# Kernel optimization log

Hardware: AMD Instinct MI355X
Metric: run time of the kernel (lower is better)

## Reference

```python
import jax, jax.numpy as jnp
import numpy as np
from jax import lax

B, Hs, Ws = 2, 256, 256
DIM = 256        # query channels (c)
DIM_BAK = 256    # key/value channels (c2)
HEADS = 8
WIN = 8
HEAD_DIM = DIM // HEADS
SCALE = HEAD_DIM ** -0.5


def window_partition(x, ws):
    # x: [B, H, W, C] -> [B*nH*nW, ws, ws, C]
    b, h, w, c = x.shape
    x = x.reshape(b, h // ws, ws, w // ws, ws, c)
    return x.transpose(0, 1, 3, 2, 4, 5).reshape(-1, ws, ws, c)


def window_reverse(windows, ws, h, w):
    # windows: [B*nH*nW, ws, ws, C] -> [B, H, W, C]
    b = windows.shape[0] // ((h // ws) * (w // ws))
    x = windows.reshape(b, h // ws, w // ws, ws, ws, -1)
    return x.transpose(0, 1, 3, 2, 4, 5).reshape(b, h, w, -1)


def setup_inputs() -> dict:
    key = jax.random.key(0)
    ks = jax.random.split(key, 9)
    s = 0.02
    return {
        "query_feature": jax.random.normal(ks[0], (B, DIM, Hs, Ws), jnp.float32),
        "key_value_feature": jax.random.normal(ks[1], (B, DIM_BAK, Hs, Ws), jnp.float32),
        # depthwise 3x3 conv on kv (groups=DIM_BAK, bias=False): OIHW with I=1
        "w_dw": jax.random.normal(ks[2], (DIM_BAK, 1, 3, 3), jnp.float32) * s,
        # to_q: Linear(dim -> dim), stored [in, out]
        "wq": jax.random.normal(ks[3], (DIM, DIM), jnp.float32) * s,
        "bq": jax.random.normal(ks[4], (DIM,), jnp.float32) * s,
        # to_kv: Linear(dim_bak -> 2*dim)
        "wkv": jax.random.normal(ks[5], (DIM_BAK, 2 * DIM), jnp.float32) * s,
        "bkv": jax.random.normal(ks[6], (2 * DIM,), jnp.float32) * s,
        # project_out: Linear(dim -> dim)
        "w_proj": jax.random.normal(ks[7], (DIM, DIM), jnp.float32) * s,
        "b_proj": jax.random.normal(ks[8], (DIM,), jnp.float32) * s,
    }


def reference(query_feature, key_value_feature, w_dw, wq, bq, wkv, bkv, w_proj, b_proj):
    b, c, h, w = query_feature.shape
    c2 = key_value_feature.shape[1]

    # depthwise 3x3 conv on key/value feature (padding=1, stride=1)
    kv = lax.conv_general_dilated(
        key_value_feature, w_dw,
        window_strides=(1, 1), padding="SAME",
        feature_group_count=c2,
        dimension_numbers=("NCHW", "OIHW", "NCHW"))

    # NCHW -> NHWC, partition into non-overlapping windows
    qw = window_partition(query_feature.transpose(0, 2, 3, 1), WIN)  # [B_, ws, ws, c]
    kvw = window_partition(kv.transpose(0, 2, 3, 1), WIN)            # [B_, ws, ws, c2]
    B_ = qw.shape[0]
    N = WIN * WIN
    qw = qw.reshape(B_, N, c)
    kvw = kvw.reshape(B_, N, c2)

    # projections -> multi-head [B_, heads, N, head_dim]
    q = (qw @ wq + bq).reshape(B_, N, HEADS, HEAD_DIM).transpose(0, 2, 1, 3) * SCALE
    kv_proj = (kvw @ wkv + bkv).reshape(B_, N, 2, HEADS, HEAD_DIM)
    k = kv_proj[:, :, 0].transpose(0, 2, 1, 3)
    v = kv_proj[:, :, 1].transpose(0, 2, 1, 3)

    # windowed cross-attention
    attn = jax.nn.softmax(jnp.einsum("bhnd,bhmd->bhnm", q, k), axis=-1)
    out = jnp.einsum("bhnm,bhmd->bhnd", attn, v)
    out = out.transpose(0, 2, 1, 3).reshape(B_, N, c)
    out = out @ w_proj + b_proj

    # reverse windows, back to NCHW
    out = window_reverse(out.reshape(B_, WIN, WIN, c), WIN, h, w)
    return out.transpose(0, 3, 1, 2)
```

## Files before the change

### kernel.cpp

```cpp
#include <hip/hip_runtime.h>
#include <hip/hip_bf16.h>
#include <cstdint>
#include <cstddef>

typedef __hip_bfloat16 bf16;
typedef short bf16x8 __attribute__((ext_vector_type(8)));
typedef float f32x4 __attribute__((ext_vector_type(4)));

#define MFMA(a, b, c) __builtin_amdgcn_mfma_f32_16x16x32_bf16((a), (b), (c), 0, 0, 0)

__global__ __launch_bounds__(256) void wtrans_k(const float* __restrict__ wq,
                                                const float* __restrict__ wkv,
                                                const float* __restrict__ wp,
                                                bf16* __restrict__ wqT,
                                                bf16* __restrict__ wkvT,
                                                bf16* __restrict__ wpT) {
  int idx = blockIdx.x * 256 + threadIdx.x;
  if (idx < 65536) {
    int n = idx >> 8, k = idx & 255;
    wqT[idx] = __float2bfloat16(wq[k * 256 + n]);
  } else if (idx < 196608) {
    int i = idx - 65536;
    int n = i >> 8, k = i & 255;
    wkvT[i] = __float2bfloat16(wkv[k * 512 + n]);
  } else {
    int i = idx - 196608;
    int n = i >> 8, k = i & 255;
    wpT[i] = __float2bfloat16(wp[k * 256 + n]);
  }
}

__global__ __launch_bounds__(256) void t_winq_k(const float* __restrict__ src,
                                                bf16* __restrict__ dst,
                                                int hw0, int swoff) {
  __shared__ bf16 T[64][66];
  int tile = blockIdx.x;
  int c0 = (tile & 3) << 6;
  int hwb = hw0 + ((tile >> 2) << 6);
  int tid = threadIdx.x;
  {
    int hwl = tid & 63, cb = tid >> 6;
    const float* s = src + (size_t)(c0 + cb) * 65536 + hwb + hwl;
#pragma unroll
    for (int i = 0; i < 16; ++i)
      T[cb + i * 4][hwl] = __float2bfloat16(s[(size_t)i * 4 * 65536]);
  }
  __syncthreads();
  {
    int cl = tid & 63, hb = tid >> 6;
#pragma unroll
    for (int j = 0; j < 16; ++j) {
      int hwl = hb + j * 4;
      int hw = hwb + hwl;
      int h = hw >> 8, w = hw & 255;
      int sw = swoff + ((h >> 3) << 5) + (w >> 3);
      int t = ((h & 7) << 3) + (w & 7);
      dst[((size_t)(sw * 64 + t) << 8) + c0 + cl] = T[cl][hwl];
    }
  }
}

__global__ __launch_bounds__(256) void t_nhwc_k(const float* __restrict__ src,
                                                bf16* __restrict__ dst) {
  __shared__ bf16 T[64][66];
  int tile = blockIdx.x;
  int c0 = (tile & 3) << 6;
  int hwoff = (tile >> 2) << 6;
  int tid = threadIdx.x;
  {
    int hwl = tid & 63, cb = tid >> 6;
    const float* s = src + (size_t)(c0 + cb) * 65536 + hwoff + hwl;
#pragma unroll
    for (int i = 0; i < 16; ++i)
      T[cb + i * 4][hwl] = __float2bfloat16(s[(size_t)i * 4 * 65536]);
  }
  __syncthreads();
  {
    int cl = tid & 63, hb = tid >> 6;
#pragma unroll
    for (int j = 0; j < 16; ++j) {
      int hwl = hb + j * 4;
      dst[((size_t)(hwoff + hwl) << 8) + c0 + cl] = T[cl][hwl];
    }
  }
}

__global__ __launch_bounds__(256) void convkv_k(const bf16* __restrict__ SK,
                                                const float* __restrict__ wdw,
                                                const bf16* __restrict__ wkvT,
                                                const float* __restrict__ bkv,
                                                bf16* __restrict__ k_s,
                                                bf16* __restrict__ vT_s,
                                                int wid_base, int cnt, int psw0,
                                                int nwtot) {
  __shared__ __align__(16) bf16 X[64 * 256];
  auto xp = [&](int row, int col) -> bf16* {
    int by = (row << 9) + (col << 1);
    by ^= (row & 7) << 4;
    return (bf16*)((char*)X + by);
  };
  int bid = blockIdx.x;
  int swc = (bid & 7) * (cnt >> 3) + (bid >> 3);
  int sw = psw0 + swc;
  int wid = wid_base + swc;
  int rem = wid & 1023, wh = rem >> 5, ww = rem & 31;
  int h0 = wh * 8, w0 = ww * 8;
  int tid = threadIdx.x;
  {
    int c = tid;
    float wr[9];
#pragma unroll
    for (int q = 0; q < 9; ++q) wr[q] = wdw[c * 9 + q];
    const bool wlo = (w0 > 0), whi = (w0 < 248);
    float rows[3][10];
    auto load_row = [&](int gh, float* r) {
      if (gh >= 0 && gh < 256) {
        const bf16* rp = SK + ((size_t)(gh * 256 + w0) << 8) + c;
        r[0] = wlo ? __bfloat162float(rp[-256]) : 0.f;
#pragma unroll
        for (int s = 1; s <= 8; ++s) r[s] = __bfloat162float(rp[(s - 1) * 256]);
        r[9] = whi ? __bfloat162float(rp[8 * 256]) : 0.f;
      } else {
#pragma unroll
        for (int e = 0; e < 10; ++e) r[e] = 0.f;
      }
    };
    load_row(h0 - 1, rows[0]);
    load_row(h0, rows[1]);
#pragma unroll
    for (int i = 0; i < 8; ++i) {
      load_row(h0 + i + 1, rows[(i + 2) % 3]);
#pragma unroll
      for (int j = 0; j < 8; ++j) {
        float acc = 0.f;
#pragma unroll
        for (int di = 0; di < 3; ++di) {
          const float* rp = rows[(i + di) % 3];
          acc = __builtin_fmaf(wr[di * 3 + 0], rp[j], acc);
          acc = __builtin_fmaf(wr[di * 3 + 1], rp[j + 1], acc);
          acc = __builtin_fmaf(wr[di * 3 + 2], rp[j + 2], acc);
        }
        *xp(i * 8 + j, c) = __float2bfloat16(acc);
      }
    }
  }
  __syncthreads();
  int wave = tid >> 6, lane = tid & 63, quad = lane >> 4, l16 = lane & 15;
  int n0 = wave * 64;
  f32x4 zero4 = {0.f, 0.f, 0.f, 0.f};
  f32x4 acc[4][4];
  for (int mt = 0; mt < 4; ++mt)
    for (int nt = 0; nt < 4; ++nt) acc[mt][nt] = zero4;
  for (int k0 = 0; k0 < 256; k0 += 32) {
    bf16x8 a[4], bb[4];
    for (int mt = 0; mt < 4; ++mt)
      a[mt] = *(const bf16x8*)xp(mt * 16 + l16, k0 + quad * 8);
    for (int nt = 0; nt < 4; ++nt)
      bb[nt] = *(const bf16x8*)&wkvT[(size_t)(n0 + nt * 16 + l16) * 256 + k0 + quad * 8];
    for (int mt = 0; mt < 4; ++mt)
      for (int nt = 0; nt < 4; ++nt) acc[mt][nt] = MFMA(a[mt], bb[nt], acc[mt][nt]);
  }
  for (int nt = 0; nt < 4; ++nt) {
    int n = n0 + nt * 16 + l16;
    float bias = bkv[n];
    for (int mt = 0; mt < 4; ++mt) {
      int mb = mt * 16 + quad * 4;
      for (int r = 0; r < 4; ++r)
        k_s[((size_t)(sw * 64 + mb + r) << 8) + n] =
            __float2bfloat16(acc[mt][nt][r] + bias);
    }
  }
  for (int mt = 0; mt < 4; ++mt)
    for (int nt = 0; nt < 4; ++nt) acc[mt][nt] = zero4;
  for (int k0 = 0; k0 < 256; k0 += 32) {
    bf16x8 a[4], bb[4];
    for (int mt = 0; mt < 4; ++mt)
      a[mt] = *(const bf16x8*)xp(mt * 16 + l16, k0 + quad * 8);
    for (int nt = 0; nt < 4; ++nt)
      bb[nt] = *(const bf16x8*)&wkvT[(size_t)(256 + n0 + nt * 16 + l16) * 256 + k0 + quad * 8];
    for (int mt = 0; mt < 4; ++mt)
      for (int nt = 0; nt < 4; ++nt) acc[mt][nt] = MFMA(bb[nt], a[mt], acc[mt][nt]);
  }
  for (int nt = 0; nt < 4; ++nt) {
    for (int r = 0; r < 4; ++r) {
      int vd = n0 + nt * 16 + quad * 4 + r;
      float bias = bkv[256 + vd];
      for (int mt = 0; mt < 4; ++mt)
        vT_s[((size_t)(sw * 256 + vd) << 6) + mt * 16 + l16] =
            __float2bfloat16(acc[mt][nt][r] + bias);
    }
  }
}

__global__ __launch_bounds__(256, 3) void fused_k(const bf16* __restrict__ qwM,
                                                  const bf16* __restrict__ wqT,
                                                  const float* __restrict__ bq,
                                                  const bf16* __restrict__ k_s,
                                                  const bf16* __restrict__ vT_s,
                                                  const bf16* __restrict__ wpT,
                                                  const float* __restrict__ bp,
                                                  float* __restrict__ out,
                                                  int wid_base, int nw) {
  __shared__ __align__(16) bf16 LA[4 * 64 * 64];
  __shared__ __align__(16) bf16 LB[4 * 64 * 32];
  int bid = blockIdx.x;
  int sw = (bid & 7) * (nw >> 3) + (bid >> 3);
  int wid = wid_base + sw;
  int b = wid >> 10, rem = wid & 1023, wh = rem >> 5, ww = rem & 31;
  int h0 = wh * 8, w0 = ww * 8;
  int tid = threadIdx.x, wave = tid >> 6, lane = tid & 63, quad = lane >> 4, l16 = lane & 15;
  char* Abase = (char*)LA + wave * 8192;
  char* Bbase = (char*)LB + wave * 4096;
  auto apR = [&](int w, int row, int col) -> bf16* {
    int by = (row << 7) + (col << 1);
    by ^= (row & 7) << 4;
    return (bf16*)((char*)LA + w * 8192 + by);
  };
  auto ap = [&](int row, int col) -> bf16* {
    int by = (row << 7) + (col << 1);
    by ^= (row & 7) << 4;
    return (bf16*)(Abase + by);
  };
  auto Bp = [&](int row, int col) -> bf16* {
    int by = (row << 6) + (col << 1);
    by ^= (row & 3) << 4;
    return (bf16*)(Bbase + by);
  };
  f32x4 zero4 = {0.f, 0.f, 0.f, 0.f};
  {
    const bf16* Aq = qwM + ((size_t)sw << 14);
    f32x4 acc[4][4];
    for (int mt = 0; mt < 4; ++mt)
      for (int nt = 0; nt < 4; ++nt) acc[mt][nt] = zero4;
    for (int k0 = 0; k0 < 256; k0 += 32) {
      bf16x8 a[4], bb[4];
      for (int mt = 0; mt < 4; ++mt)
        a[mt] = *(const bf16x8*)&Aq[(size_t)(mt * 16 + l16) * 256 + k0 + quad * 8];
      for (int nt = 0; nt < 4; ++nt) {
        int n = (wave + ((nt >> 1) << 2)) * 32 + (nt & 1) * 16 + l16;
        bb[nt] = *(const bf16x8*)&wqT[(size_t)n * 256 + k0 + quad * 8];
      }
      for (int mt = 0; mt < 4; ++mt)
        for (int nt = 0; nt < 4; ++nt) acc[mt][nt] = MFMA(a[mt], bb[nt], acc[mt][nt]);
    }
    const float scale = 0.1767766952966369f;
    for (int nt = 0; nt < 4; ++nt) {
      int n = (wave + ((nt >> 1) << 2)) * 32 + (nt & 1) * 16 + l16;
      float bias = bq[n];
      for (int mt = 0; mt < 4; ++mt) {
        int mb = mt * 16 + quad * 4;
        for (int r = 0; r < 4; ++r)
          *ap(mb + r, nt * 16 + l16) =
              __float2bfloat16((acc[mt][nt][r] + bias) * scale);
      }
    }
  }
  const bf16* kw = k_s + ((size_t)sw << 14);
  const bf16* vw = vT_s + ((size_t)sw << 14);
  for (int hi = 0; hi < 2; ++hi) {
    int co = (wave + hi * 4) * 32;
    int lc = hi * 32;
    f32x4 s[4][4];
    for (int mt = 0; mt < 4; ++mt)
      for (int nt = 0; nt < 4; ++nt) s[mt][nt] = zero4;
    {
      bf16x8 a[4], bb[4];
      for (int mt = 0; mt < 4; ++mt)
        a[mt] = *(const bf16x8*)ap(mt * 16 + l16, lc + quad * 8);
      for (int nt = 0; nt < 4; ++nt)
        bb[nt] = *(const bf16x8*)&kw[(size_t)(nt * 16 + l16) * 256 + co + quad * 8];
      for (int mt = 0; mt < 4; ++mt)
        for (int nt = 0; nt < 4; ++nt) s[mt][nt] = MFMA(a[mt], bb[nt], s[mt][nt]);
    }
    float rsum[4][4];
    for (int mt = 0; mt < 4; ++mt) {
      for (int r = 0; r < 4; ++r) {
        float m = s[mt][0][r];
        for (int nt = 1; nt < 4; ++nt) m = fmaxf(m, s[mt][nt][r]);
        m = fmaxf(m, __shfl_xor(m, 1, 64));
        m = fmaxf(m, __shfl_xor(m, 2, 64));
        m = fmaxf(m, __shfl_xor(m, 4, 64));
        m = fmaxf(m, __shfl_xor(m, 8, 64));
        float sum = 0.f;
        for (int nt = 0; nt < 4; ++nt) {
          float e = __expf(s[mt][nt][r] - m);
          s[mt][nt][r] = e;
          sum += e;
        }
        sum += __shfl_xor(sum, 1, 64);
        sum += __shfl_xor(sum, 2, 64);
        sum += __shfl_xor(sum, 4, 64);
        sum += __shfl_xor(sum, 8, 64);
        rsum[mt][r] = sum;
      }
    }
    f32x4 o[4][2];
    for (int mt = 0; mt < 4; ++mt)
      for (int nt = 0; nt < 2; ++nt) o[mt][nt] = zero4;
    for (int half = 0; half < 2; ++half) {
      for (int mt = 0; mt < 4; ++mt)
        for (int nt2 = 0; nt2 < 2; ++nt2)
          for (int r = 0; r < 4; ++r)
            *Bp(mt * 16 + quad * 4 + r, nt2 * 16 + l16) =
                __float2bfloat16(s[mt][half * 2 + nt2][r]);
      bf16x8 pa[4], vb[2];
      for (int mt = 0; mt < 4; ++mt)
        pa[mt] = *(const bf16x8*)Bp(mt * 16 + l16, quad * 8);
      for (int nt = 0; nt < 2; ++nt)
        vb[nt] = *(const bf16x8*)&vw[(size_t)(co + nt * 16 + l16) * 64 + half * 32 + quad * 8];
      for (int mt = 0; mt < 4; ++mt)
        for (int nt = 0; nt < 2; ++nt) o[mt][nt] = MFMA(pa[mt], vb[nt], o[mt][nt]);
    }
    for (int mt = 0; mt < 4; ++mt) {
      int mb = mt * 16 + quad * 4;
      for (int nt = 0; nt < 2; ++nt)
        for (int r = 0; r < 4; ++r)
          *ap(mb + r, lc + nt * 16 + l16) =
              __float2bfloat16(o[mt][nt][r] / rsum[mt][r]);
    }
  }
  __syncthreads();
  {
    int n0 = wave * 64;
    f32x4 acc[4][4];
    for (int mt = 0; mt < 4; ++mt)
      for (int nt = 0; nt < 4; ++nt) acc[mt][nt] = zero4;
    for (int k0 = 0; k0 < 256; k0 += 32) {
      int head = k0 >> 5;
      int rw = head & 3;
      int lc = (head >> 2) * 32;
      bf16x8 a[4], bb[4];
      for (int mt = 0; mt < 4; ++mt)
        a[mt] = *(const bf16x8*)apR(rw, mt * 16 + l16, lc + quad * 8);
      for (int nt = 0; nt < 4; ++nt)
        bb[nt] = *(const bf16x8*)&wpT[(size_t)(n0 + nt * 16 + l16) * 256 + k0 + quad * 8];
      for (int mt = 0; mt < 4; ++mt)
        for (int nt = 0; nt < 4; ++nt) acc[mt][nt] = MFMA(a[mt], bb[nt], acc[mt][nt]);
    }
    for (int nt = 0; nt < 4; ++nt) {
      int n = n0 + nt * 16 + l16;
      float bias = bp[n];
      float* chan = out + ((size_t)(b * 256 + n) << 16);
      for (int mt = 0; mt < 4; ++mt) {
        int row_i = mt * 2 + (quad >> 1);
        int j0 = (quad & 1) * 4;
        f32x4 v4;
        for (int r = 0; r < 4; ++r) v4[r] = acc[mt][nt][r] + bias;
        *(f32x4*)&chan[(size_t)(h0 + row_i) * 256 + w0 + j0] = v4;
      }
    }
  }
}

extern "C" void kernel_launch(void* const* d_in, const int* in_sizes, int n_in,
                              void* d_out, int out_size, void* d_ws, size_t ws_size,
                              hipStream_t stream) {
  const float* qf  = (const float*)d_in[0];
  const float* kvf = (const float*)d_in[1];
  const float* wdw = (const float*)d_in[2];
  const float* wq  = (const float*)d_in[3];
  const float* bq  = (const float*)d_in[4];
  const float* wkv = (const float*)d_in[5];
  const float* bkv = (const float*)d_in[6];
  const float* wp  = (const float*)d_in[7];
  const float* bp  = (const float*)d_in[8];
  float* out = (float*)d_out;

  bf16* wqT  = (bf16*)d_ws;
  bf16* wkvT = wqT + 65536;
  bf16* wpT  = wkvT + 131072;
  bf16* bufs = wpT + 65536;
  const size_t welems = 65536 + 131072 + 65536;
  const size_t skelems = (size_t)256 * 256 * 256;

  int passes = 1;
  while (passes < 32) {
    size_t nw_ = 2048 / passes;
    size_t elems = welems + skelems + 3 * nw_ * 16384;
    if (elems * 2 <= ws_size) break;
    passes <<= 1;
  }
  int nw = 2048 / passes;
  size_t sz = (size_t)nw * 16384;
  bf16* SK  = bufs;
  bf16* qwM = SK + skelems;
  bf16* KS  = qwM + sz;
  bf16* VT  = KS + sz;

  wtrans_k<<<1024, 256, 0, stream>>>(wq, wkv, wp, wqT, wkvT, wpT);

  for (int p = 0; p < passes; ++p) {
    int wbP = p * nw;
    int b0 = wbP >> 10, b1 = (wbP + nw - 1) >> 10;
    for (int b = b0; b <= b1; ++b) {
      int s = wbP > b * 1024 ? wbP : b * 1024;
      int e = (wbP + nw) < (b + 1) * 1024 ? (wbP + nw) : (b + 1) * 1024;
      int cnt = e - s;
      int h0 = ((s & 1023) >> 5) * 8;
      t_winq_k<<<cnt * 4, 256, 0, stream>>>(qf + ((size_t)b << 24), qwM,
                                            h0 * 256, b * 1024 - wbP);
    }
    for (int b = b0; b <= b1; ++b) {
      int s = wbP > b * 1024 ? wbP : b * 1024;
      int e = (wbP + nw) < (b + 1) * 1024 ? (wbP + nw) : (b + 1) * 1024;
      int cnt = e - s;
      t_nhwc_k<<<4096, 256, 0, stream>>>(kvf + ((size_t)b << 24), SK);
      convkv_k<<<cnt, 256, 0, stream>>>(SK, wdw, wkvT, bkv, KS, VT,
                                        s, cnt, s - wbP, nw);
    }
    fused_k<<<nw, 256, 0, stream>>>(qwM, wqT, bq, KS, VT, wpT, bp, out, wbP, nw);
  }
}
```

Baseline: 623.5 us.

## Stage Q window into LDS via async global_load_lds and prefetch K/V fragments

The 64x256 query window tile is copied into a new 32KB swizzled LDS buffer with global_load_lds at kernel start. The K and V fragments for both head groups are loaded into registers up front, overlapping with that copy. The separate P scratch buffer is dropped in favour of reusing the per-wave LA region. This aims to hide global-load latency behind the Q projection and cut scattered global reads. In exchange, more LDS and more registers are used, and launch bounds drop from 3 to 2 blocks per CU, which lowers occupancy.

```diff
diff --git a/kernel.cpp b/kernel.cpp
--- a/kernel.cpp
+++ b/kernel.cpp
@@ -192,7 +192,7 @@
   }
 }
 
-__global__ __launch_bounds__(256, 3) void fused_k(const bf16* __restrict__ qwM,
+__global__ __launch_bounds__(256, 2) void fused_k(const bf16* __restrict__ qwM,
                                                   const bf16* __restrict__ wqT,
                                                   const float* __restrict__ bq,
                                                   const bf16* __restrict__ k_s,
@@ -201,41 +201,71 @@
                                                   const float* __restrict__ bp,
                                                   float* __restrict__ out,
                                                   int wid_base, int nw) {
+  __shared__ __align__(16) bf16 XQ[64 * 256];
   __shared__ __align__(16) bf16 LA[4 * 64 * 64];
-  __shared__ __align__(16) bf16 LB[4 * 64 * 32];
   int bid = blockIdx.x;
   int sw = (bid & 7) * (nw >> 3) + (bid >> 3);
   int wid = wid_base + sw;
   int b = wid >> 10, rem = wid & 1023, wh = rem >> 5, ww = rem & 31;
   int h0 = wh * 8, w0 = ww * 8;
   int tid = threadIdx.x, wave = tid >> 6, lane = tid & 63, quad = lane >> 4, l16 = lane & 15;
+  const bf16* kw = k_s + ((size_t)sw << 14);
+  const bf16* vw = vT_s + ((size_t)sw << 14);
+
+  {
+    const char* Aq = (const char*)(qwM + ((size_t)sw << 14));
+#pragma unroll
+    for (int rr = 0; rr < 8; ++rr) {
+      int L = rr * 4096 + wave * 1024 + lane * 16;
+      int gl = L ^ (((L >> 9) & 7) << 4);
+      __builtin_amdgcn_global_load_lds(
+          (const __attribute__((address_space(1))) void*)(Aq + gl),
+          (__attribute__((address_space(3))) void*)((char*)XQ + rr * 4096 + wave * 1024),
+          16, 0, 0);
+    }
+  }
+  bf16x8 kfr[2][4], vfr[2][2][2];
+#pragma unroll
+  for (int hi = 0; hi < 2; ++hi) {
+    int co = (wave + hi * 4) * 32;
+#pragma unroll
+    for (int nt = 0; nt < 4; ++nt)
+      kfr[hi][nt] = *(const bf16x8*)&kw[(size_t)(nt * 16 + l16) * 256 + co + quad * 8];
+#pragma unroll
+    for (int half = 0; half < 2; ++half)
+#pragma unroll
+      for (int nt = 0; nt < 2; ++nt)
+        vfr[hi][half][nt] =
+            *(const bf16x8*)&vw[(size_t)(co + nt * 16 + l16) * 64 + half * 32 + quad * 8];
+  }
+  __syncthreads();
+
+  auto xq = [&](int row, int col) -> const bf16* {
+    int by = (row << 9) + (col << 1);
+    by ^= (row & 7) << 4;
+    return (const bf16*)((const char*)XQ + by);
+  };
   char* Abase = (char*)LA + wave * 8192;
-  char* Bbase = (char*)LB + wave * 4096;
+  auto ap = [&](int row, int col) -> bf16* {
+    int by = (row << 7) + (col << 1);
+    by ^= (row & 7) << 4;
+    return (bf16*)(Abase + by);
+  };
   auto apR = [&](int w, int row, int col) -> bf16* {
     int by = (row << 7) + (col << 1);
     by ^= (row & 7) << 4;
     return (bf16*)((char*)LA + w * 8192 + by);
   };
-  auto ap = [&](int row, int col) -> bf16* {
-    int by = (row << 7) + (col << 1);
-    by ^= (row & 7) << 4;
-    return (bf16*)(Abase + by);
-  };
-  auto Bp = [&](int row, int col) -> bf16* {
-    int by = (row << 6) + (col << 1);
-    by ^= (row & 3) << 4;
-    return (bf16*)(Bbase + by);
-  };
   f32x4 zero4 = {0.f, 0.f, 0.f, 0.f};
-  {
-    const bf16* Aq = qwM + ((size_t)sw << 14);
+
+  {
     f32x4 acc[4][4];
     for (int mt = 0; mt < 4; ++mt)
       for (int nt = 0; nt < 4; ++nt) acc[mt][nt] = zero4;
     for (int k0 = 0; k0 < 256; k0 += 32) {
       bf16x8 a[4], bb[4];
       for (int mt = 0; mt < 4; ++mt)
-        a[mt] = *(const bf16x8*)&Aq[(size_t)(mt * 16 + l16) * 256 + k0 + quad * 8];
+        a[mt] = *(const bf16x8*)xq(mt * 16 + l16, k0 + quad * 8);
       for (int nt = 0; nt < 4; ++nt) {
         int n = (wave + ((nt >> 1) << 2)) * 32 + (nt & 1) * 16 + l16;
         bb[nt] = *(const bf16x8*)&wqT[(size_t)n * 256 + k0 + quad * 8];
@@ -255,22 +285,19 @@
       }
     }
   }
-  const bf16* kw = k_s + ((size_t)sw << 14);
-  const bf16* vw = vT_s + ((size_t)sw << 14);
+#pragma unroll
   for (int hi = 0; hi < 2; ++hi) {
-    int co = (wave + hi * 4) * 32;
     int lc = hi * 32;
     f32x4 s[4][4];
     for (int mt = 0; mt < 4; ++mt)
       for (int nt = 0; nt < 4; ++nt) s[mt][nt] = zero4;
     {
-      bf16x8 a[4], bb[4];
+      bf16x8 a[4];
       for (int mt = 0; mt < 4; ++mt)
         a[mt] = *(const bf16x8*)ap(mt * 16 + l16, lc + quad * 8);
-      for (int nt = 0; nt < 4; ++nt)
-        bb[nt] = *(const bf16x8*)&kw[(size_t)(nt * 16 + l16) * 256 + co + quad * 8];
-      for (int mt = 0; mt < 4; ++mt)
-        for (int nt = 0; nt < 4; ++nt) s[mt][nt] = MFMA(a[mt], bb[nt], s[mt][nt]);
+      for (int mt = 0; mt < 4; ++mt)
+#pragma unroll
+        for (int nt = 0; nt < 4; ++nt) s[mt][nt] = MFMA(a[mt], kfr[hi][nt], s[mt][nt]);
     }
     float rsum[4][4];
     for (int mt = 0; mt < 4; ++mt) {
@@ -297,19 +324,21 @@
     f32x4 o[4][2];
     for (int mt = 0; mt < 4; ++mt)
       for (int nt = 0; nt < 2; ++nt) o[mt][nt] = zero4;
+#pragma unroll
     for (int half = 0; half < 2; ++half) {
       for (int mt = 0; mt < 4; ++mt)
+#pragma unroll
         for (int nt2 = 0; nt2 < 2; ++nt2)
           for (int r = 0; r < 4; ++r)
-            *Bp(mt * 16 + quad * 4 + r, nt2 * 16 + l16) =
+            *ap(mt * 16 + quad * 4 + r, lc + nt2 * 16 + l16) =
                 __float2bfloat16(s[mt][half * 2 + nt2][r]);
-      bf16x8 pa[4], vb[2];
-      for (int mt = 0; mt < 4; ++mt)
-        pa[mt] = *(const bf16x8*)Bp(mt * 16 + l16, quad * 8);
-      for (int nt = 0; nt < 2; ++nt)
-        vb[nt] = *(const bf16x8*)&vw[(size_t)(co + nt * 16 + l16) * 64 + half * 32 + quad * 8];
-      for (int mt = 0; mt < 4; ++mt)
-        for (int nt = 0; nt < 2; ++nt) o[mt][nt] = MFMA(pa[mt], vb[nt], o[mt][nt]);
+      bf16x8 pa[4];
+      for (int mt = 0; mt < 4; ++mt)
+        pa[mt] = *(const bf16x8*)ap(mt * 16 + l16, lc + quad * 8);
+      for (int mt = 0; mt < 4; ++mt)
+#pragma unroll
+        for (int nt = 0; nt < 2; ++nt)
+          o[mt][nt] = MFMA(pa[mt], vfr[hi][half][nt], o[mt][nt]);
     }
     for (int mt = 0; mt < 4; ++mt) {
       int mb = mt * 16 + quad * 4;
```

New measurement: 595.5 us. 1.05x faster.
